# Performance work log

Measured on AMD Instinct MI355X. Metric: run time of the kernel, lower is better.

Reference implementation:

```python
import jax, jax.numpy as jnp
import numpy as np

SIGMAS = [0.5, 1.0, 2.0, 4.0, 8.0]
FILTER_SIZE = int(4 * SIGMAS[-1] + 1)  # 33
PAD = int(2 * SIGMAS[-1])              # 16
K1, K2 = 0.01, 0.03
ALPHA = 0.025
COMPENSATION = 20.0
DATA_RANGE = 1.0


def _gauss_2d(size, sigma):
    coords = np.arange(size, dtype=np.float32) - size // 2
    g = np.exp(-coords ** 2 / (2.0 * sigma ** 2))
    g = g / g.sum()
    return np.outer(g, g)


def _build_g_masks():
    # [n_sigmas, 1, 33, 33] OIHW
    masks = np.stack([_gauss_2d(FILTER_SIZE, s)[None] for s in SIGMAS], axis=0)
    return jnp.asarray(masks, dtype=jnp.float32)


def setup_inputs() -> dict:
    key = jax.random.key(0)
    kx, ky = jax.random.split(key)
    x = jax.random.uniform(kx, (16, 1, 512, 512), dtype=jnp.float32)
    y = jax.random.uniform(ky, (16, 1, 512, 512), dtype=jnp.float32)
    return {"x": x, "y": y, "g_masks": _build_g_masks()}


def _conv(t, w):
    # t: [B,1,H,W], w: [O,1,33,33] -> [B,O,H,W] ('same' padding)
    return jax.lax.conv_general_dilated(
        t, w, window_strides=(1, 1), padding=[(PAD, PAD), (PAD, PAD)],
        dimension_numbers=("NCHW", "OIHW", "NCHW"))


def reference(x, y, g_masks):
    C1 = (K1 * DATA_RANGE) ** 2
    C2 = (K2 * DATA_RANGE) ** 2

    mux = _conv(x, g_masks)   # [B,5,H,W]
    muy = _conv(y, g_masks)
    mux2 = mux * mux
    muy2 = muy * muy
    muxy = mux * muy
    sigmax2 = _conv(x * x, g_masks) - mux2
    sigmay2 = _conv(y * y, g_masks) - muy2
    sigmaxy = _conv(x * y, g_masks) - muxy

    luminance = (2.0 * muxy + C1) / (mux2 + muy2 + C1)
    cs = (2.0 * sigmaxy + C2) / (sigmax2 + sigmay2 + C2)

    lM = luminance[:, -1, :, :]          # largest-scale luminance
    PIcs = jnp.prod(cs, axis=1)          # product of contrast-structure over scales
    loss_ms_ssim = 1.0 - lM * PIcs       # [B,H,W]

    loss_l1 = jnp.abs(x - y)             # [B,1,H,W]
    gaussian_l1 = _conv(loss_l1, g_masks[-1:]).mean(axis=1)  # [B,H,W]

    loss_mix = ALPHA * loss_ms_ssim + (1.0 - ALPHA) * gaussian_l1 / DATA_RANGE
    return (COMPENSATION * loss_mix).mean()
```

## Files before the change

kernel.cpp:

```cpp
#include <hip/hip_runtime.h>
#include <hip/hip_bf16.h>

namespace {

constexpr float kAlpha = 0.025f;
constexpr float kC1 = 1.0e-4f;
constexpr float kC2 = 9.0e-4f;

constexpr int MPS = 68;
constexpr int HTS = 68;

typedef __attribute__((ext_vector_type(8))) short short8;
typedef __attribute__((ext_vector_type(4))) float f32x4;

struct __align__(16) Smem {
  union {
    short mp[2][64 * MPS];
    short hbT[4][32 * HTS];
  };
  float red[4];
  int gtab[2][5][48];
};

union Frag {
  int i[4];
  short8 s8;
};

__device__ __forceinline__ unsigned f2bf(float f) {
  unsigned u = __float_as_uint(f);
  return (u + 0x7FFFu + ((u >> 16) & 1u)) >> 16;
}
__device__ __forceinline__ unsigned pk(float a, float b) {
  union {
    __hip_bfloat162 h;
    unsigned u;
  } c;
  c.h = __float22bfloat162_rn(make_float2(a, b));
  return c.u;
}
__device__ __forceinline__ float bfl(unsigned u) {
  return __uint_as_float(u << 16);
}
__device__ __forceinline__ float bfh(unsigned u) {
  return __uint_as_float(u & 0xFFFF0000u);
}
__device__ __forceinline__ float frcp(float x) {
  return __builtin_amdgcn_rcpf(x);
}

__device__ __forceinline__ short8 wbuild2(const int* tb, int nt, int kt) {
  Frag u;
#pragma unroll
  for (int j = 0; j < 4; ++j) u.i[j] = tb[16 * kt - 8 * nt + 8 + j];
  return u.s8;
}

__device__ __forceinline__ void load_xy(const Smem& sm, int row, int quad,
                                        Frag fx[2], Frag fy[2]) {
  const short* px = &sm.mp[0][row * MPS + quad * 8];
  const short* py = &sm.mp[1][row * MPS + quad * 8];
  *(int2*)&fx[0].i[0] = *(const int2*)(px);
  *(int2*)&fx[0].i[2] = *(const int2*)(px + 4);
  *(int2*)&fx[1].i[0] = *(const int2*)(px + 32);
  *(int2*)&fx[1].i[2] = *(const int2*)(px + 36);
  *(int2*)&fy[0].i[0] = *(const int2*)(py);
  *(int2*)&fy[0].i[2] = *(const int2*)(py + 4);
  *(int2*)&fy[1].i[0] = *(const int2*)(py + 32);
  *(int2*)&fy[1].i[2] = *(const int2*)(py + 36);
}

__global__ __launch_bounds__(256, 6) void msssim_l1_kernel(
    const float* __restrict__ x, const float* __restrict__ y,
    const float* __restrict__ gm, float* __restrict__ out) {
  __shared__ Smem sm;
  const int tid = threadIdx.x;
  const int lane = tid & 63;
  const int w = tid >> 6;
  const int quad = lane >> 4;
  const int l16 = lane & 15;

  float corr;
  {
    float traw4 = (lane < 33) ? gm[4 * 1089 + 528 + lane] : 0.f;
    float g = traw4 * rsqrtf(__shfl(traw4, 16, 64));
    float se = g, st = bfl(f2bf(g));
#pragma unroll
    for (int off = 32; off > 0; off >>= 1) {
      se += __shfl_xor(se, off, 64);
      st += __shfl_xor(st, off, 64);
    }
    float r1 = se / st;
    corr = r1 * r1;
  }

  {
    int* gt = &sm.gtab[0][0][0];
    for (int q = tid; q < 480; q += 256) {
      int par = q >= 240;
      int rem = par ? q - 240 : q;
      int s = rem / 48;
      int i = rem - s * 48;
      int t0 = 2 * i + par;
      const float* grow = gm + s * 1089 + 528;
      float rsc = rsqrtf(grow[16]);
      int g0 = t0 - 31, g1 = t0 - 30;
      unsigned lo = (g0 >= 0 && g0 <= 32) ? f2bf(grow[g0] * rsc) : 0u;
      unsigned hi = (g1 >= 0 && g1 <= 32) ? f2bf(grow[g1] * rsc) : 0u;
      gt[q] = (int)(lo | (hi << 16));
    }
  }

  const int D = (quad * 8 - l16 + 31) >> 1;
  const int* gD = &sm.gtab[(l16 & 1) ? 0 : 1][0][0] + D - 8;

  const float* xb = x + blockIdx.z * (512 * 512);
  const float* yb = y + blockIdx.z * (512 * 512);
  const int rb = blockIdx.y * 32 - 16;
  const int cb = blockIdx.x * 32 - 16;
  for (int f = tid; f < 1024; f += 256) {
    int pr = f >> 4;
    int pc = (f & 15) << 2;
    int gr = rb + pr, gc = cb + pc;
    float4 vx = make_float4(0.f, 0.f, 0.f, 0.f);
    float4 vy = vx;
    if (gr >= 0 && gr < 512 && gc >= 0 && gc < 512) {
      vx = *(const float4*)(xb + gr * 512 + gc);
      vy = *(const float4*)(yb + gr * 512 + gc);
    }
    const int base = pr * MPS + pc;
    *(int2*)(&sm.mp[0][base]) =
        make_int2((int)pk(vx.x, vx.y), (int)pk(vx.z, vx.w));
    *(int2*)(&sm.mp[1][base]) =
        make_int2((int)pk(vy.x, vy.y), (int)pk(vy.z, vy.w));
  }
  __syncthreads();

  Frag A[4][2];
  Frag dA[2];
#pragma unroll
  for (int mt = 0; mt < 4; ++mt) {
    Frag fx[2], fy[2];
    load_xy(sm, mt * 16 + l16, quad, fx, fy);
    if (mt == w) {
#pragma unroll
      for (int h = 0; h < 2; ++h)
#pragma unroll
        for (int i = 0; i < 4; ++i) {
          unsigned ux = (unsigned)fx[h].i[i], uy = (unsigned)fy[h].i[i];
          dA[h].i[i] =
              (int)pk(fabsf(bfl(ux) - bfl(uy)), fabsf(bfh(ux) - bfh(uy)));
        }
    }
    if (w == 0) {
      A[mt][0] = fx[0];
      A[mt][1] = fx[1];
    } else if (w == 1) {
      A[mt][0] = fy[0];
      A[mt][1] = fy[1];
    } else {
#pragma unroll
      for (int h = 0; h < 2; ++h)
#pragma unroll
        for (int i = 0; i < 4; ++i) {
          unsigned ux = (unsigned)fx[h].i[i], uy = (unsigned)fy[h].i[i];
          float xl = bfl(ux), xh = bfh(ux), yl = bfl(uy), yh = bfh(uy);
          A[mt][h].i[i] = (w == 2) ? (int)pk(fmaf(xl, xl, yl * yl),
                                            fmaf(xh, xh, yh * yh))
                                   : (int)pk(xl * yl, xh * yh);
        }
    }
  }
  __syncthreads();

  const int mtv = w >> 1, ntv = w & 1;
  f32x4 Pcs = {1.f, 1.f, 1.f, 1.f};
  f32x4 lumP = {0.f, 0.f, 0.f, 0.f};
  f32x4 l1v = {0.f, 0.f, 0.f, 0.f};

#pragma unroll
  for (int s = 0; s < 5; ++s) {
    const int* tb = gD + s * 48;
    short8 wf[2][2];
#pragma unroll
    for (int nt = 0; nt < 2; ++nt)
#pragma unroll
      for (int kt = 0; kt < 2; ++kt) wf[nt][kt] = wbuild2(tb, nt, kt);
#pragma unroll
    for (int mt = 0; mt < 4; ++mt)
#pragma unroll
      for (int nt = 0; nt < 2; ++nt) {
        f32x4 acc = {0.f, 0.f, 0.f, 0.f};
        acc = __builtin_amdgcn_mfma_f32_16x16x32_bf16(A[mt][0].s8, wf[nt][0],
                                                      acc, 0, 0, 0);
        acc = __builtin_amdgcn_mfma_f32_16x16x32_bf16(A[mt][1].s8, wf[nt][1],
                                                      acc, 0, 0, 0);
        *(int2*)(&sm.hbT[w][(nt * 16 + l16) * HTS + mt * 16 + quad * 4]) =
            make_int2((int)pk(acc[0], acc[1]), (int)pk(acc[2], acc[3]));
      }
    __syncthreads();

    short8 wa0 = wbuild2(tb, mtv, 0);
    short8 wa1 = wbuild2(tb, mtv, 1);
    f32x4 va[4];
#pragma unroll
    for (int m = 0; m < 4; ++m) {
      const short* bp = &sm.hbT[m][(ntv * 16 + l16) * HTS + quad * 8];
      Frag b0, b1;
      *(int2*)&b0.i[0] = *(const int2*)(bp);
      *(int2*)&b0.i[2] = *(const int2*)(bp + 4);
      *(int2*)&b1.i[0] = *(const int2*)(bp + 32);
      *(int2*)&b1.i[2] = *(const int2*)(bp + 36);
      f32x4 acc = {0.f, 0.f, 0.f, 0.f};
      acc = __builtin_amdgcn_mfma_f32_16x16x32_bf16(wa0, b0.s8, acc, 0, 0, 0);
      acc = __builtin_amdgcn_mfma_f32_16x16x32_bf16(wa1, b1.s8, acc, 0, 0, 0);
      va[m] = acc;
    }
#pragma unroll
    for (int r = 0; r < 4; ++r) {
      float mux = va[0][r], muy = va[1][r], m2 = va[2][r], mxy = va[3][r];
      float mux2 = mux * mux, muy2 = muy * muy, muxy = mux * muy;
      float cs = (2.f * (mxy - muxy) + kC2) * frcp((m2 - mux2 - muy2) + kC2);
      Pcs[r] *= cs;
      if (s == 4)
        lumP[r] = ((2.f * muxy + kC1) * frcp(mux2 + muy2 + kC1)) * Pcs[r];
    }
    __syncthreads();
  }

  {
    const int* tb = gD + 4 * 48;
    short8 wf[2][2];
#pragma unroll
    for (int nt = 0; nt < 2; ++nt)
#pragma unroll
      for (int kt = 0; kt < 2; ++kt) wf[nt][kt] = wbuild2(tb, nt, kt);
#pragma unroll
    for (int nt = 0; nt < 2; ++nt) {
      f32x4 acc = {0.f, 0.f, 0.f, 0.f};
      acc = __builtin_amdgcn_mfma_f32_16x16x32_bf16(dA[0].s8, wf[nt][0], acc,
                                                    0, 0, 0);
      acc = __builtin_amdgcn_mfma_f32_16x16x32_bf16(dA[1].s8, wf[nt][1], acc,
                                                    0, 0, 0);
      *(int2*)(&sm.hbT[0][(nt * 16 + l16) * HTS + w * 16 + quad * 4]) =
          make_int2((int)pk(acc[0], acc[1]), (int)pk(acc[2], acc[3]));
    }
    __syncthreads();

    short8 wa0 = wbuild2(tb, mtv, 0);
    short8 wa1 = wbuild2(tb, mtv, 1);
    const short* bp = &sm.hbT[0][(ntv * 16 + l16) * HTS + quad * 8];
    Frag b0, b1;
    *(int2*)&b0.i[0] = *(const int2*)(bp);
    *(int2*)&b0.i[2] = *(const int2*)(bp + 4);
    *(int2*)&b1.i[0] = *(const int2*)(bp + 32);
    *(int2*)&b1.i[2] = *(const int2*)(bp + 36);
    f32x4 acc = {0.f, 0.f, 0.f, 0.f};
    acc = __builtin_amdgcn_mfma_f32_16x16x32_bf16(wa0, b0.s8, acc, 0, 0, 0);
    acc = __builtin_amdgcn_mfma_f32_16x16x32_bf16(wa1, b1.s8, acc, 0, 0, 0);
#pragma unroll
    for (int r = 0; r < 4; ++r) l1v[r] = acc[r] * corr;
  }

  float lsum = 0.f;
#pragma unroll
  for (int r = 0; r < 4; ++r)
    lsum += kAlpha * (1.f - lumP[r]) + (1.f - kAlpha) * l1v[r];
#pragma unroll
  for (int off = 32; off > 0; off >>= 1) lsum += __shfl_down(lsum, off, 64);
  if ((tid & 63) == 0) sm.red[tid >> 6] = lsum;
  __syncthreads();
  if (tid == 0) {
    float t = sm.red[0] + sm.red[1] + sm.red[2] + sm.red[3];
    atomicAdd(out, t * (20.f / (16.f * 512.f * 512.f)));
  }
}

}

extern "C" void kernel_launch(void* const* d_in, const int* in_sizes, int n_in,
                              void* d_out, int out_size, void* d_ws,
                              size_t ws_size, hipStream_t stream) {
  (void)in_sizes;
  (void)n_in;
  (void)d_ws;
  (void)ws_size;
  (void)out_size;
  const float* x = (const float*)d_in[0];
  const float* y = (const float*)d_in[1];
  const float* gm = (const float*)d_in[2];
  float* out = (float*)d_out;
  hipMemsetAsync(out, 0, sizeof(float), stream);
  dim3 grid(16, 16, 16);
  msssim_l1_kernel<<<grid, dim3(256), 0, stream>>>(x, y, gm, out);
}
```

Measured before the change: 150.2 us.

## Precompute L1 horizontal pass early, stream SSIM epilogue, relax launch bounds

The horizontal MFMA pass for the Gaussian-L1 term now runs before the scale loop and keeps its packed results in registers (l1h), so dA can be freed early. The final pass only writes those values to shared memory. The weight fragments are built per nt instead of all four at once. The SSIM math is folded into the vertical-pass loop so the four accumulators are not all kept live. Launch bounds drop from 6 to 4 waves per EU, which allows more registers per thread in exchange for lower occupancy.

Measured after the change: 148.4 us. No clear change (-1.2%).

```diff
diff --git a/kernel.cpp b/kernel.cpp
--- a/kernel.cpp
+++ b/kernel.cpp
@@ -70,7 +70,7 @@
   *(int2*)&fy[1].i[2] = *(const int2*)(py + 36);
 }
 
-__global__ __launch_bounds__(256, 6) void msssim_l1_kernel(
+__global__ __launch_bounds__(256, 4) void msssim_l1_kernel(
     const float* __restrict__ x, const float* __restrict__ y,
     const float* __restrict__ gm, float* __restrict__ out) {
   __shared__ Smem sm;
@@ -171,6 +171,22 @@
         }
     }
   }
+
+  int2 l1h[2];
+  {
+    const int* tb = gD + 4 * 48;
+#pragma unroll
+    for (int nt = 0; nt < 2; ++nt) {
+      short8 w0 = wbuild2(tb, nt, 0);
+      short8 w1 = wbuild2(tb, nt, 1);
+      f32x4 acc = {0.f, 0.f, 0.f, 0.f};
+      acc = __builtin_amdgcn_mfma_f32_16x16x32_bf16(dA[0].s8, w0, acc, 0, 0,
+                                                    0);
+      acc = __builtin_amdgcn_mfma_f32_16x16x32_bf16(dA[1].s8, w1, acc, 0, 0,
+                                                    0);
+      l1h[nt] = make_int2((int)pk(acc[0], acc[1]), (int)pk(acc[2], acc[3]));
+    }
+  }
   __syncthreads();
 
   const int mtv = w >> 1, ntv = w & 1;
@@ -181,28 +197,26 @@
 #pragma unroll
   for (int s = 0; s < 5; ++s) {
     const int* tb = gD + s * 48;
-    short8 wf[2][2];
-#pragma unroll
-    for (int nt = 0; nt < 2; ++nt)
-#pragma unroll
-      for (int kt = 0; kt < 2; ++kt) wf[nt][kt] = wbuild2(tb, nt, kt);
-#pragma unroll
-    for (int mt = 0; mt < 4; ++mt)
-#pragma unroll
-      for (int nt = 0; nt < 2; ++nt) {
+#pragma unroll
+    for (int nt = 0; nt < 2; ++nt) {
+      short8 w0 = wbuild2(tb, nt, 0);
+      short8 w1 = wbuild2(tb, nt, 1);
+#pragma unroll
+      for (int mt = 0; mt < 4; ++mt) {
         f32x4 acc = {0.f, 0.f, 0.f, 0.f};
-        acc = __builtin_amdgcn_mfma_f32_16x16x32_bf16(A[mt][0].s8, wf[nt][0],
-                                                      acc, 0, 0, 0);
-        acc = __builtin_amdgcn_mfma_f32_16x16x32_bf16(A[mt][1].s8, wf[nt][1],
-                                                      acc, 0, 0, 0);
+        acc = __builtin_amdgcn_mfma_f32_16x16x32_bf16(A[mt][0].s8, w0, acc, 0,
+                                                      0, 0);
+        acc = __builtin_amdgcn_mfma_f32_16x16x32_bf16(A[mt][1].s8, w1, acc, 0,
+                                                      0, 0);
         *(int2*)(&sm.hbT[w][(nt * 16 + l16) * HTS + mt * 16 + quad * 4]) =
             make_int2((int)pk(acc[0], acc[1]), (int)pk(acc[2], acc[3]));
       }
+    }
     __syncthreads();
 
     short8 wa0 = wbuild2(tb, mtv, 0);
     short8 wa1 = wbuild2(tb, mtv, 1);
-    f32x4 va[4];
+    f32x4 mux, muy, T;
 #pragma unroll
     for (int m = 0; m < 4; ++m) {
       const short* bp = &sm.hbT[m][(ntv * 16 + l16) * HTS + quad * 8];
@@ -214,37 +228,36 @@
       f32x4 acc = {0.f, 0.f, 0.f, 0.f};
       acc = __builtin_amdgcn_mfma_f32_16x16x32_bf16(wa0, b0.s8, acc, 0, 0, 0);
       acc = __builtin_amdgcn_mfma_f32_16x16x32_bf16(wa1, b1.s8, acc, 0, 0, 0);
-      va[m] = acc;
-    }
-#pragma unroll
-    for (int r = 0; r < 4; ++r) {
-      float mux = va[0][r], muy = va[1][r], m2 = va[2][r], mxy = va[3][r];
-      float mux2 = mux * mux, muy2 = muy * muy, muxy = mux * muy;
-      float cs = (2.f * (mxy - muxy) + kC2) * frcp((m2 - mux2 - muy2) + kC2);
-      Pcs[r] *= cs;
-      if (s == 4)
-        lumP[r] = ((2.f * muxy + kC1) * frcp(mux2 + muy2 + kC1)) * Pcs[r];
+      if (m == 0) {
+        mux = acc;
+      } else if (m == 1) {
+        muy = acc;
+      } else if (m == 2) {
+#pragma unroll
+        for (int r = 0; r < 4; ++r)
+          T[r] = (acc[r] - mux[r] * mux[r]) - muy[r] * muy[r];
+      } else {
+#pragma unroll
+        for (int r = 0; r < 4; ++r) {
+          float cs =
+              (2.f * (acc[r] - mux[r] * muy[r]) + kC2) * frcp(T[r] + kC2);
+          Pcs[r] *= cs;
+          if (s == 4)
+            lumP[r] = ((2.f * (mux[r] * muy[r]) + kC1) *
+                       frcp((mux[r] * mux[r] + muy[r] * muy[r]) + kC1)) *
+                      Pcs[r];
+        }
+      }
     }
     __syncthreads();
   }
 
   {
     const int* tb = gD + 4 * 48;
-    short8 wf[2][2];
 #pragma unroll
     for (int nt = 0; nt < 2; ++nt)
-#pragma unroll
-      for (int kt = 0; kt < 2; ++kt) wf[nt][kt] = wbuild2(tb, nt, kt);
-#pragma unroll
-    for (int nt = 0; nt < 2; ++nt) {
-      f32x4 acc = {0.f, 0.f, 0.f, 0.f};
-      acc = __builtin_amdgcn_mfma_f32_16x16x32_bf16(dA[0].s8, wf[nt][0], acc,
-                                                    0, 0, 0);
-      acc = __builtin_amdgcn_mfma_f32_16x16x32_bf16(dA[1].s8, wf[nt][1], acc,
-                                                    0, 0, 0);
       *(int2*)(&sm.hbT[0][(nt * 16 + l16) * HTS + w * 16 + quad * 4]) =
-          make_int2((int)pk(acc[0], acc[1]), (int)pk(acc[2], acc[3]));
-    }
+          l1h[nt];
     __syncthreads();
 
     short8 wa0 = wbuild2(tb, mtv, 0);
```
